# Performance work log

Hardware: AMD Instinct MI355X
Metric: run time of the kernel (lower is better)

Reference implementation:

```python
import jax, jax.numpy as jnp
import numpy as np

B, S, N, U, E, L = 32, 32, 128, 64, 2, 2
N_STEPS = 3
NUM_CLASSES = 5


def setup_inputs() -> dict:
    key = jax.random.key(0)
    ks = jax.random.split(key, 10)
    input_seq = jax.random.normal(ks[0], (B, S, N * U), dtype=jnp.float32)
    seq_lengths = jax.random.randint(ks[1], (B,), 0, S)
    # per-edge-type adjacency, scaled ~row-stochastic for numerical sanity
    adjacency_matrix = jax.random.uniform(ks[2], (B, E, N, N), dtype=jnp.float32) / N
    sc = 1.0 / np.sqrt(U)
    W_msg = jax.random.normal(ks[3], (L, E, U, U), dtype=jnp.float32) * sc
    b_msg = jnp.zeros((L, U), dtype=jnp.float32)
    Wg = jax.random.normal(ks[4], (L, 3, U, U), dtype=jnp.float32) * sc  # gates from aggregated messages
    Ug = jax.random.normal(ks[5], (L, 3, U, U), dtype=jnp.float32) * sc  # gates from hidden state
    bg = jnp.zeros((L, 3, U), dtype=jnp.float32)
    fc_w = jax.random.normal(ks[6], (U, NUM_CLASSES), dtype=jnp.float32) * sc
    fc_b = jnp.zeros((NUM_CLASSES,), dtype=jnp.float32)
    return {
        "input_seq": input_seq, "seq_lengths": seq_lengths,
        "adjacency_matrix": adjacency_matrix,
        "W_msg": W_msg, "b_msg": b_msg, "Wg": Wg, "Ug": Ug, "bg": bg,
        "fc_w": fc_w, "fc_b": fc_b,
    }


def _ggnn_layer(h, A, W_msg_l, b_msg_l, Wg_l, Ug_l, bg_l):
    # h: [S,B,N,U], A: [B,E,N,N] (shared across timesteps)
    for _ in range(N_STEPS):
        # typed message passing: sum_e A_e @ h @ W_e
        a = jnp.einsum('benm,sbmu,euv->sbnv', A, h, W_msg_l) + b_msg_l
        g_a = jnp.einsum('sbnu,guv->gsbnv', a, Wg_l)  # [3,S,B,N,U]
        z = jax.nn.sigmoid(g_a[0] + h @ Ug_l[0] + bg_l[0])
        r = jax.nn.sigmoid(g_a[1] + h @ Ug_l[1] + bg_l[1])
        c = jnp.tanh(g_a[2] + (r * h) @ Ug_l[2] + bg_l[2])
        h = (1.0 - z) * h + z * c
    return h


def reference(input_seq, seq_lengths, adjacency_matrix, W_msg, b_msg, Wg, Ug, bg, fc_w, fc_b):
    # encoder: hidden state is NOT carried across timesteps in the original
    # (cell is called with current input only), so timesteps are vectorized.
    cur = input_seq.reshape(B, S, N, U).transpose(1, 0, 2, 3)  # [S,B,N,U]
    for l in range(L):
        cur = _ggnn_layer(cur, adjacency_matrix, W_msg[l], b_msg[l], Wg[l], Ug[l], bg[l])
    out = cur.transpose(1, 0, 2, 3)  # [B,S,N,U]
    idx = jnp.clip(seq_lengths - 1, 0, S - 1)
    last = out[jnp.arange(B), idx]  # [B,N,U] (last relevant timestep)
    # dropout is identity in eval mode
    logits = jax.nn.relu(last) @ fc_w + fc_b  # [B,N,C]
    return jnp.max(logits, axis=1)  # [B,C]
```

## Files before the change

kernel.cpp:

```cpp
#include <hip/hip_runtime.h>

#define B 32
#define S 32
#define N 128
#define U 64
#define E 2
#define NCLS 5
#define RPW 4


__device__ __forceinline__ float sigmoid_f(float x) {
    return __fdividef(1.f, 1.f + __expf(-x));
}
__device__ __forceinline__ float tanh_f(float x) {
    float t = __expf(-2.f * fabsf(x));
    float y = __fdividef(1.f - t, 1.f + t);
    return copysignf(y, x);
}
__device__ __forceinline__ float bcast(float v, int u) {
    return __uint_as_float(__builtin_amdgcn_readlane(__float_as_uint(v), u));
}

template <int FIRST, int LAST>
__global__ __launch_bounds__(256) void k_step(
    const float* __restrict__ x, const int* __restrict__ lens,
    const float* __restrict__ hin, float* __restrict__ hout,
    const float* __restrict__ A, const float* __restrict__ Wmsg,
    const float* __restrict__ bmsg, const float* __restrict__ Wg,
    const float* __restrict__ Ug, const float* __restrict__ bg,
    const float* __restrict__ fcw, float* __restrict__ partial, int l) {
    __shared__ float red[4 * NCLS];
    int tid = threadIdx.x;
    int wave = tid >> 6, lane = tid & 63;
    int b = blockIdx.x >> 3;
    int q = blockIdx.x & 7;
    int n0 = __builtin_amdgcn_readfirstlane(q * 16 + wave * RPW);

    const float* __restrict__ hsrc;
    if (FIRST) {
        int idx = lens[b] - 1;
        idx = idx < 0 ? 0 : (idx > S - 1 ? S - 1 : idx);
        hsrc = x + (size_t)(b * S + idx) * N * U;
    } else {
        hsrc = hin + (size_t)b * N * U;
    }

    float hv[RPW];
#pragma unroll
    for (int r = 0; r < RPW; ++r) hv[r] = hsrc[(n0 + r) * U + lane];

    float s[RPW][E];
#pragma unroll
    for (int r = 0; r < RPW; ++r) { s[r][0] = 0.f; s[r][1] = 0.f; }
    {
        const float4* Ap[E][RPW];
#pragma unroll
        for (int e = 0; e < E; ++e)
#pragma unroll
            for (int r = 0; r < RPW; ++r)
                Ap[e][r] = (const float4*)(A + (((size_t)b * E + e) * N + n0 + r) * N);
#pragma unroll 2
        for (int m4 = 0; m4 < N / 4; ++m4) {
            float q0 = hsrc[(m4 * 4 + 0) * U + lane];
            float q1 = hsrc[(m4 * 4 + 1) * U + lane];
            float q2 = hsrc[(m4 * 4 + 2) * U + lane];
            float q3 = hsrc[(m4 * 4 + 3) * U + lane];
#pragma unroll
            for (int e = 0; e < E; ++e)
#pragma unroll
                for (int r = 0; r < RPW; ++r) {
                    float4 a = Ap[e][r][m4];
                    s[r][e] = fmaf(a.x, q0, s[r][e]);
                    s[r][e] = fmaf(a.y, q1, s[r][e]);
                    s[r][e] = fmaf(a.z, q2, s[r][e]);
                    s[r][e] = fmaf(a.w, q3, s[r][e]);
                }
        }
    }

    float bm = bmsg[l * U + lane];
    float av[RPW];
#pragma unroll
    for (int r = 0; r < RPW; ++r) av[r] = bm;
    {
        const float* W0 = Wmsg + (size_t)(l * E + 0) * U * U + lane;
        const float* W1 = W0 + U * U;
#pragma unroll 16
        for (int u = 0; u < U; ++u) {
            float w = W0[u * U];
#pragma unroll
            for (int r = 0; r < RPW; ++r) av[r] = fmaf(bcast(s[r][0], u), w, av[r]);
        }
#pragma unroll 16
        for (int u = 0; u < U; ++u) {
            float w = W1[u * U];
#pragma unroll
            for (int r = 0; r < RPW; ++r) av[r] = fmaf(bcast(s[r][1], u), w, av[r]);
        }
    }

    const float* Wg0 = Wg + (size_t)l * 3 * U * U + lane;
    const float* Wg1 = Wg0 + U * U;
    const float* Wg2 = Wg1 + U * U;
    const float* Ug0 = Ug + (size_t)l * 3 * U * U + lane;
    const float* Ug1 = Ug0 + U * U;
    const float* Ug2 = Ug1 + U * U;
    float bz = bg[(l * 3 + 0) * U + lane];
    float br = bg[(l * 3 + 1) * U + lane];
    float bcc = bg[(l * 3 + 2) * U + lane];
    float accz[RPW], accr[RPW], accc[RPW];
#pragma unroll
    for (int r = 0; r < RPW; ++r) { accz[r] = bz; accr[r] = br; accc[r] = bcc; }
#pragma unroll 8
    for (int u = 0; u < U; ++u) {
        float w0 = Wg0[u * U], w1 = Wg1[u * U], w2 = Wg2[u * U];
        float g0 = Ug0[u * U], g1 = Ug1[u * U];
#pragma unroll
        for (int r = 0; r < RPW; ++r) {
            float a = bcast(av[r], u);
            float h = bcast(hv[r], u);
            accz[r] = fmaf(a, w0, accz[r]); accz[r] = fmaf(h, g0, accz[r]);
            accr[r] = fmaf(a, w1, accr[r]); accr[r] = fmaf(h, g1, accr[r]);
            accc[r] = fmaf(a, w2, accc[r]);
        }
    }
    float rh[RPW];
#pragma unroll
    for (int r = 0; r < RPW; ++r) rh[r] = sigmoid_f(accr[r]) * hv[r];
#pragma unroll 16
    for (int u = 0; u < U; ++u) {
        float g2 = Ug2[u * U];
#pragma unroll
        for (int r = 0; r < RPW; ++r) accc[r] = fmaf(bcast(rh[r], u), g2, accc[r]);
    }
    float hn[RPW];
#pragma unroll
    for (int r = 0; r < RPW; ++r) {
        float zg = sigmoid_f(accz[r]);
        hn[r] = (1.f - zg) * hv[r] + zg * tanh_f(accc[r]);
    }

    if (!LAST) {
#pragma unroll
        for (int r = 0; r < RPW; ++r)
            hout[((size_t)b * N + n0 + r) * U + lane] = hn[r];
    } else {
        float lg[RPW][NCLS];
#pragma unroll
        for (int r = 0; r < RPW; ++r) {
            float rv = hn[r] > 0.f ? hn[r] : 0.f;
#pragma unroll
            for (int c = 0; c < NCLS; ++c) lg[r][c] = rv * fcw[lane * NCLS + c];
        }
#pragma unroll
        for (int off = 32; off; off >>= 1)
#pragma unroll
            for (int r = 0; r < RPW; ++r)
#pragma unroll
                for (int c = 0; c < NCLS; ++c) lg[r][c] += __shfl_xor(lg[r][c], off, 64);
        if (lane == 0) {
#pragma unroll
            for (int c = 0; c < NCLS; ++c)
                red[wave * NCLS + c] =
                    fmaxf(fmaxf(lg[0][c], lg[1][c]), fmaxf(lg[2][c], lg[3][c]));
        }
        __syncthreads();
        if (tid < NCLS) {
            float m = red[tid];
            for (int w = 1; w < 4; ++w) m = fmaxf(m, red[w * NCLS + tid]);
            partial[(size_t)(b * 8 + q) * NCLS + tid] = m;
        }
    }
}

__global__ void k_final(const float* __restrict__ partial, const float* __restrict__ fcb,
                        float* __restrict__ out) {
    int b = blockIdx.x, c = threadIdx.x;
    if (c < NCLS) {
        float m = -3.4e38f;
        for (int jj = 0; jj < 8; ++jj)
            m = fmaxf(m, partial[(size_t)(b * 8 + jj) * NCLS + c]);
        out[b * NCLS + c] = m + fcb[c];
    }
}

extern "C" void kernel_launch(void* const* d_in, const int* in_sizes, int n_in,
                              void* d_out, int out_size, void* d_ws, size_t ws_size,
                              hipStream_t stream) {
    const float* x    = (const float*)d_in[0];
    const int*   lens = (const int*)d_in[1];
    const float* A    = (const float*)d_in[2];
    const float* Wmsg = (const float*)d_in[3];
    const float* bmsg = (const float*)d_in[4];
    const float* Wg   = (const float*)d_in[5];
    const float* Ug   = (const float*)d_in[6];
    const float* bg   = (const float*)d_in[7];
    const float* fcw  = (const float*)d_in[8];
    const float* fcb  = (const float*)d_in[9];
    float* out = (float*)d_out;

    float* hA      = (float*)d_ws;
    float* hB      = hA + (size_t)B * N * U;
    float* partial = hB + (size_t)B * N * U;

    k_step<1, 0><<<B * 8, 256, 0, stream>>>(x, lens, nullptr, hA, A, Wmsg, bmsg, Wg, Ug, bg, fcw, partial, 0);
    k_step<0, 0><<<B * 8, 256, 0, stream>>>(x, lens, hA, hB, A, Wmsg, bmsg, Wg, Ug, bg, fcw, partial, 0);
    k_step<0, 0><<<B * 8, 256, 0, stream>>>(x, lens, hB, hA, A, Wmsg, bmsg, Wg, Ug, bg, fcw, partial, 0);
    k_step<0, 0><<<B * 8, 256, 0, stream>>>(x, lens, hA, hB, A, Wmsg, bmsg, Wg, Ug, bg, fcw, partial, 1);
    k_step<0, 0><<<B * 8, 256, 0, stream>>>(x, lens, hB, hA, A, Wmsg, bmsg, Wg, Ug, bg, fcw, partial, 1);
    k_step<0, 1><<<B * 8, 256, 0, stream>>>(x, lens, hA, hB, A, Wmsg, bmsg, Wg, Ug, bg, fcw, partial, 1);
    k_final<<<B, 64, 0, stream>>>(partial, fcb, out);
}
```

Before: 225.0 us.

## Split reductions across waves with LDS combine and pre-transposed float4 weights

Each block now covers 8 node rows, and its four waves split every reduction dimension four ways: the adjacency sum over m, and the sum over u in the message and gate matmuls. Partial sums are combined through shared memory with several barriers. The grid doubles to 512 blocks, and a new prep kernel transposes the weights into float4-packed layouts so each lane can load four weights at once. This shortens each wave's serial dependency chain and adds parallelism, at the cost of LDS traffic, extra __syncthreads, and an extra launch per call.

```diff
diff --git a/kernel.cpp b/kernel.cpp
--- a/kernel.cpp
+++ b/kernel.cpp
@@ -6,7 +6,6 @@
 #define U 64
 #define E 2
 #define NCLS 5
-#define RPW 4
 
 
 __device__ __forceinline__ float sigmoid_f(float x) {
@@ -21,20 +20,39 @@
     return __uint_as_float(__builtin_amdgcn_readlane(__float_as_uint(v), u));
 }
 
+__global__ __launch_bounds__(256) void k_prep(
+    const float* __restrict__ Wmsg, const float* __restrict__ Wg,
+    const float* __restrict__ Ug, float4* __restrict__ wt) {
+    int m = blockIdx.x;
+    const float* src;
+    if (m < 4)       src = Wmsg + (size_t)m * U * U;
+    else if (m < 10) src = Wg + (size_t)(m - 4) * U * U;
+    else             src = Ug + (size_t)(m - 10) * U * U;
+    for (int i = threadIdx.x; i < (U / 4) * U; i += 256) {
+        int u4 = i >> 6, v = i & 63;
+        wt[(size_t)m * 1024 + i] =
+            make_float4(src[(u4 * 4 + 0) * U + v], src[(u4 * 4 + 1) * U + v],
+                        src[(u4 * 4 + 2) * U + v], src[(u4 * 4 + 3) * U + v]);
+    }
+}
+
 template <int FIRST, int LAST>
-__global__ __launch_bounds__(256) void k_step(
+__global__ __launch_bounds__(256, 4) void k_step(
     const float* __restrict__ x, const int* __restrict__ lens,
     const float* __restrict__ hin, float* __restrict__ hout,
-    const float* __restrict__ A, const float* __restrict__ Wmsg,
-    const float* __restrict__ bmsg, const float* __restrict__ Wg,
-    const float* __restrict__ Ug, const float* __restrict__ bg,
+    const float* __restrict__ A, const float4* __restrict__ wt,
+    const float* __restrict__ bmsg, const float* __restrict__ bg,
     const float* __restrict__ fcw, float* __restrict__ partial, int l) {
-    __shared__ float red[4 * NCLS];
+    __shared__ float sA[4][8][2][64];
+    __shared__ float sB[4][8][64];
+    __shared__ float sC[4][8][64];
     int tid = threadIdx.x;
-    int wave = tid >> 6, lane = tid & 63;
-    int b = blockIdx.x >> 3;
-    int q = blockIdx.x & 7;
-    int n0 = __builtin_amdgcn_readfirstlane(q * 16 + wave * RPW);
+    int k = __builtin_amdgcn_readfirstlane(tid >> 6);
+    int lane = tid & 63;
+    int b = blockIdx.x >> 4;
+    int j = blockIdx.x & 15;
+    int n0 = __builtin_amdgcn_readfirstlane(j * 8);
+    int m0 = __builtin_amdgcn_readfirstlane(k * 32);
 
     const float* __restrict__ hsrc;
     if (FIRST) {
@@ -45,130 +63,200 @@
         hsrc = hin + (size_t)b * N * U;
     }
 
-    float hv[RPW];
-#pragma unroll
-    for (int r = 0; r < RPW; ++r) hv[r] = hsrc[(n0 + r) * U + lane];
-
-    float s[RPW][E];
-#pragma unroll
-    for (int r = 0; r < RPW; ++r) { s[r][0] = 0.f; s[r][1] = 0.f; }
+    float hv[8];
+#pragma unroll
+    for (int r = 0; r < 8; ++r) hv[r] = hsrc[(n0 + r) * U + lane];
+
+    float s2[8][2];
+#pragma unroll
+    for (int e = 0; e < E; ++e) {
+        float acc[8];
+#pragma unroll
+        for (int r = 0; r < 8; ++r) acc[r] = 0.f;
+        const float4* Ap[8];
+#pragma unroll
+        for (int r = 0; r < 8; ++r)
+            Ap[r] = (const float4*)(A + (((size_t)b * E + e) * N + n0 + r) * N + m0);
+#pragma unroll 2
+        for (int m4 = 0; m4 < 8; ++m4) {
+            float q0 = hsrc[(m0 + m4 * 4 + 0) * U + lane];
+            float q1 = hsrc[(m0 + m4 * 4 + 1) * U + lane];
+            float q2 = hsrc[(m0 + m4 * 4 + 2) * U + lane];
+            float q3 = hsrc[(m0 + m4 * 4 + 3) * U + lane];
+#pragma unroll
+            for (int r = 0; r < 8; ++r) {
+                float4 a = Ap[r][m4];
+                acc[r] = fmaf(a.x, q0, acc[r]);
+                acc[r] = fmaf(a.y, q1, acc[r]);
+                acc[r] = fmaf(a.z, q2, acc[r]);
+                acc[r] = fmaf(a.w, q3, acc[r]);
+            }
+        }
+#pragma unroll
+        for (int r = 0; r < 8; ++r) s2[r][e] = acc[r];
+    }
+#pragma unroll
+    for (int r = 0; r < 8; ++r) {
+        sA[k][r][0][lane] = s2[r][0];
+        sA[k][r][1][lane] = s2[r][1];
+    }
+    __syncthreads();
+#pragma unroll
+    for (int r = 0; r < 8; ++r) {
+        s2[r][0] = (sA[0][r][0][lane] + sA[1][r][0][lane]) + (sA[2][r][0][lane] + sA[3][r][0][lane]);
+        s2[r][1] = (sA[0][r][1][lane] + sA[1][r][1][lane]) + (sA[2][r][1][lane] + sA[3][r][1][lane]);
+    }
+
+    float av[8];
     {
-        const float4* Ap[E][RPW];
-#pragma unroll
-        for (int e = 0; e < E; ++e)
-#pragma unroll
-            for (int r = 0; r < RPW; ++r)
-                Ap[e][r] = (const float4*)(A + (((size_t)b * E + e) * N + n0 + r) * N);
-#pragma unroll 2
-        for (int m4 = 0; m4 < N / 4; ++m4) {
-            float q0 = hsrc[(m4 * 4 + 0) * U + lane];
-            float q1 = hsrc[(m4 * 4 + 1) * U + lane];
-            float q2 = hsrc[(m4 * 4 + 2) * U + lane];
-            float q3 = hsrc[(m4 * 4 + 3) * U + lane];
-#pragma unroll
-            for (int e = 0; e < E; ++e)
-#pragma unroll
-                for (int r = 0; r < RPW; ++r) {
-                    float4 a = Ap[e][r][m4];
-                    s[r][e] = fmaf(a.x, q0, s[r][e]);
-                    s[r][e] = fmaf(a.y, q1, s[r][e]);
-                    s[r][e] = fmaf(a.z, q2, s[r][e]);
-                    s[r][e] = fmaf(a.w, q3, s[r][e]);
+        float bm = (k == 0) ? bmsg[l * U + lane] : 0.f;
+#pragma unroll
+        for (int r = 0; r < 8; ++r) av[r] = bm;
+        const float4* W0t = wt + (size_t)(l * E + 0) * 1024 + lane;
+        const float4* W1t = W0t + 1024;
+#pragma unroll
+        for (int u4 = 0; u4 < 4; ++u4) {
+            float4 w4 = W0t[(k * 4 + u4) * 64];
+#pragma unroll
+            for (int i = 0; i < 4; ++i) {
+                int u = k * 16 + u4 * 4 + i;
+                float wv = ((const float*)&w4)[i];
+#pragma unroll
+                for (int r = 0; r < 8; ++r) av[r] = fmaf(bcast(s2[r][0], u), wv, av[r]);
+            }
+        }
+#pragma unroll
+        for (int u4 = 0; u4 < 4; ++u4) {
+            float4 w4 = W1t[(k * 4 + u4) * 64];
+#pragma unroll
+            for (int i = 0; i < 4; ++i) {
+                int u = k * 16 + u4 * 4 + i;
+                float wv = ((const float*)&w4)[i];
+#pragma unroll
+                for (int r = 0; r < 8; ++r) av[r] = fmaf(bcast(s2[r][1], u), wv, av[r]);
+            }
+        }
+    }
+#pragma unroll
+    for (int r = 0; r < 8; ++r) sB[k][r][lane] = av[r];
+    __syncthreads();
+#pragma unroll
+    for (int r = 0; r < 8; ++r)
+        av[r] = (sB[0][r][lane] + sB[1][r][lane]) + (sB[2][r][lane] + sB[3][r][lane]);
+
+    float accz[8], accr[8], accc[8];
+    {
+        float bz = (k == 0) ? bg[(l * 3 + 0) * U + lane] : 0.f;
+        float br = (k == 0) ? bg[(l * 3 + 1) * U + lane] : 0.f;
+        float bcc = (k == 0) ? bg[(l * 3 + 2) * U + lane] : 0.f;
+#pragma unroll
+        for (int r = 0; r < 8; ++r) { accz[r] = bz; accr[r] = br; accc[r] = bcc; }
+        const float4* Wg0t = wt + (size_t)(4 + l * 3 + 0) * 1024 + lane;
+        const float4* Wg1t = Wg0t + 1024;
+        const float4* Wg2t = Wg1t + 1024;
+        const float4* Ug0t = wt + (size_t)(10 + l * 3 + 0) * 1024 + lane;
+        const float4* Ug1t = Ug0t + 1024;
+#pragma unroll
+        for (int u4 = 0; u4 < 4; ++u4) {
+            float4 w0 = Wg0t[(k * 4 + u4) * 64];
+            float4 w1 = Wg1t[(k * 4 + u4) * 64];
+            float4 w2 = Wg2t[(k * 4 + u4) * 64];
+            float4 g0 = Ug0t[(k * 4 + u4) * 64];
+            float4 g1 = Ug1t[(k * 4 + u4) * 64];
+#pragma unroll
+            for (int i = 0; i < 4; ++i) {
+                int u = k * 16 + u4 * 4 + i;
+                float w0v = ((const float*)&w0)[i], w1v = ((const float*)&w1)[i];
+                float w2v = ((const float*)&w2)[i];
+                float g0v = ((const float*)&g0)[i], g1v = ((const float*)&g1)[i];
+#pragma unroll
+                for (int r = 0; r < 8; ++r) {
+                    float a = bcast(av[r], u);
+                    float h = bcast(hv[r], u);
+                    accz[r] = fmaf(a, w0v, accz[r]); accz[r] = fmaf(h, g0v, accz[r]);
+                    accr[r] = fmaf(a, w1v, accr[r]); accr[r] = fmaf(h, g1v, accr[r]);
+                    accc[r] = fmaf(a, w2v, accc[r]);
                 }
-        }
-    }
-
-    float bm = bmsg[l * U + lane];
-    float av[RPW];
-#pragma unroll
-    for (int r = 0; r < RPW; ++r) av[r] = bm;
+            }
+        }
+    }
+#pragma unroll
+    for (int r = 0; r < 8; ++r) {
+        sA[k][r][0][lane] = accz[r];
+        sA[k][r][1][lane] = accr[r];
+        sC[k][r][lane] = accc[r];
+    }
+    __syncthreads();
+#pragma unroll
+    for (int r = 0; r < 8; ++r) {
+        accz[r] = (sA[0][r][0][lane] + sA[1][r][0][lane]) + (sA[2][r][0][lane] + sA[3][r][0][lane]);
+        accr[r] = (sA[0][r][1][lane] + sA[1][r][1][lane]) + (sA[2][r][1][lane] + sA[3][r][1][lane]);
+        accc[r] = (sC[0][r][lane] + sC[1][r][lane]) + (sC[2][r][lane] + sC[3][r][lane]);
+    }
+
+    float rh[8];
+#pragma unroll
+    for (int r = 0; r < 8; ++r) rh[r] = sigmoid_f(accr[r]) * hv[r];
     {
-        const float* W0 = Wmsg + (size_t)(l * E + 0) * U * U + lane;
-        const float* W1 = W0 + U * U;
-#pragma unroll 16
-        for (int u = 0; u < U; ++u) {
-            float w = W0[u * U];
-#pragma unroll
-            for (int r = 0; r < RPW; ++r) av[r] = fmaf(bcast(s[r][0], u), w, av[r]);
-        }
-#pragma unroll 16
-        for (int u = 0; u < U; ++u) {
-            float w = W1[u * U];
-#pragma unroll
-            for (int r = 0; r < RPW; ++r) av[r] = fmaf(bcast(s[r][1], u), w, av[r]);
-        }
-    }
-
-    const float* Wg0 = Wg + (size_t)l * 3 * U * U + lane;
-    const float* Wg1 = Wg0 + U * U;
-    const float* Wg2 = Wg1 + U * U;
-    const float* Ug0 = Ug + (size_t)l * 3 * U * U + lane;
-    const float* Ug1 = Ug0 + U * U;
-    const float* Ug2 = Ug1 + U * U;
-    float bz = bg[(l * 3 + 0) * U + lane];
-    float br = bg[(l * 3 + 1) * U + lane];
-    float bcc = bg[(l * 3 + 2) * U + lane];
-    float accz[RPW], accr[RPW], accc[RPW];
-#pragma unroll
-    for (int r = 0; r < RPW; ++r) { accz[r] = bz; accr[r] = br; accc[r] = bcc; }
-#pragma unroll 8
-    for (int u = 0; u < U; ++u) {
-        float w0 = Wg0[u * U], w1 = Wg1[u * U], w2 = Wg2[u * U];
-        float g0 = Ug0[u * U], g1 = Ug1[u * U];
-#pragma unroll
-        for (int r = 0; r < RPW; ++r) {
-            float a = bcast(av[r], u);
-            float h = bcast(hv[r], u);
-            accz[r] = fmaf(a, w0, accz[r]); accz[r] = fmaf(h, g0, accz[r]);
-            accr[r] = fmaf(a, w1, accr[r]); accr[r] = fmaf(h, g1, accr[r]);
-            accc[r] = fmaf(a, w2, accc[r]);
-        }
-    }
-    float rh[RPW];
-#pragma unroll
-    for (int r = 0; r < RPW; ++r) rh[r] = sigmoid_f(accr[r]) * hv[r];
-#pragma unroll 16
-    for (int u = 0; u < U; ++u) {
-        float g2 = Ug2[u * U];
-#pragma unroll
-        for (int r = 0; r < RPW; ++r) accc[r] = fmaf(bcast(rh[r], u), g2, accc[r]);
-    }
-    float hn[RPW];
-#pragma unroll
-    for (int r = 0; r < RPW; ++r) {
+        const float4* Ug2t = wt + (size_t)(10 + l * 3 + 2) * 1024 + lane;
+        float c2[8];
+#pragma unroll
+        for (int r = 0; r < 8; ++r) c2[r] = 0.f;
+#pragma unroll
+        for (int u4 = 0; u4 < 4; ++u4) {
+            float4 g2 = Ug2t[(k * 4 + u4) * 64];
+#pragma unroll
+            for (int i = 0; i < 4; ++i) {
+                int u = k * 16 + u4 * 4 + i;
+                float g2v = ((const float*)&g2)[i];
+#pragma unroll
+                for (int r = 0; r < 8; ++r) c2[r] = fmaf(bcast(rh[r], u), g2v, c2[r]);
+            }
+        }
+#pragma unroll
+        for (int r = 0; r < 8; ++r) sB[k][r][lane] = c2[r];
+    }
+    __syncthreads();
+#pragma unroll
+    for (int r = 0; r < 8; ++r)
+        accc[r] += (sB[0][r][lane] + sB[1][r][lane]) + (sB[2][r][lane] + sB[3][r][lane]);
+
+    float hn[8];
+#pragma unroll
+    for (int r = 0; r < 8; ++r) {
         float zg = sigmoid_f(accz[r]);
         hn[r] = (1.f - zg) * hv[r] + zg * tanh_f(accc[r]);
     }
 
     if (!LAST) {
-#pragma unroll
-        for (int r = 0; r < RPW; ++r)
-            hout[((size_t)b * N + n0 + r) * U + lane] = hn[r];
+        if (k == 0) {
+#pragma unroll
+            for (int r = 0; r < 8; ++r)
+                hout[((size_t)b * N + n0 + r) * U + lane] = hn[r];
+        }
     } else {
-        float lg[RPW][NCLS];
-#pragma unroll
-        for (int r = 0; r < RPW; ++r) {
-            float rv = hn[r] > 0.f ? hn[r] : 0.f;
-#pragma unroll
-            for (int c = 0; c < NCLS; ++c) lg[r][c] = rv * fcw[lane * NCLS + c];
-        }
-#pragma unroll
-        for (int off = 32; off; off >>= 1)
-#pragma unroll
-            for (int r = 0; r < RPW; ++r)
-#pragma unroll
-                for (int c = 0; c < NCLS; ++c) lg[r][c] += __shfl_xor(lg[r][c], off, 64);
-        if (lane == 0) {
-#pragma unroll
-            for (int c = 0; c < NCLS; ++c)
-                red[wave * NCLS + c] =
-                    fmaxf(fmaxf(lg[0][c], lg[1][c]), fmaxf(lg[2][c], lg[3][c]));
-        }
-        __syncthreads();
-        if (tid < NCLS) {
-            float m = red[tid];
-            for (int w = 1; w < 4; ++w) m = fmaxf(m, red[w * NCLS + tid]);
-            partial[(size_t)(b * 8 + q) * NCLS + tid] = m;
+        if (k == 0) {
+            float mc[NCLS];
+#pragma unroll
+            for (int c = 0; c < NCLS; ++c) mc[c] = -3.4e38f;
+#pragma unroll
+            for (int r = 0; r < 8; ++r) {
+                float rv = hn[r] > 0.f ? hn[r] : 0.f;
+                float lg[NCLS];
+#pragma unroll
+                for (int c = 0; c < NCLS; ++c) lg[c] = rv * fcw[lane * NCLS + c];
+#pragma unroll
+                for (int off = 32; off; off >>= 1)
+#pragma unroll
+                    for (int c = 0; c < NCLS; ++c) lg[c] += __shfl_xor(lg[c], off, 64);
+#pragma unroll
+                for (int c = 0; c < NCLS; ++c) mc[c] = fmaxf(mc[c], lg[c]);
+            }
+            if (lane == 0) {
+#pragma unroll
+                for (int c = 0; c < NCLS; ++c)
+                    partial[(size_t)(b * 16 + j) * NCLS + c] = mc[c];
+            }
         }
     }
 }
@@ -178,8 +266,8 @@
     int b = blockIdx.x, c = threadIdx.x;
     if (c < NCLS) {
         float m = -3.4e38f;
-        for (int jj = 0; jj < 8; ++jj)
-            m = fmaxf(m, partial[(size_t)(b * 8 + jj) * NCLS + c]);
+        for (int jj = 0; jj < 16; ++jj)
+            m = fmaxf(m, partial[(size_t)(b * 16 + jj) * NCLS + c]);
         out[b * NCLS + c] = m + fcb[c];
     }
 }
@@ -202,12 +290,14 @@
     float* hA      = (float*)d_ws;
     float* hB      = hA + (size_t)B * N * U;
     float* partial = hB + (size_t)B * N * U;
-
-    k_step<1, 0><<<B * 8, 256, 0, stream>>>(x, lens, nullptr, hA, A, Wmsg, bmsg, Wg, Ug, bg, fcw, partial, 0);
-    k_step<0, 0><<<B * 8, 256, 0, stream>>>(x, lens, hA, hB, A, Wmsg, bmsg, Wg, Ug, bg, fcw, partial, 0);
-    k_step<0, 0><<<B * 8, 256, 0, stream>>>(x, lens, hB, hA, A, Wmsg, bmsg, Wg, Ug, bg, fcw, partial, 0);
-    k_step<0, 0><<<B * 8, 256, 0, stream>>>(x, lens, hA, hB, A, Wmsg, bmsg, Wg, Ug, bg, fcw, partial, 1);
-    k_step<0, 0><<<B * 8, 256, 0, stream>>>(x, lens, hB, hA, A, Wmsg, bmsg, Wg, Ug, bg, fcw, partial, 1);
-    k_step<0, 1><<<B * 8, 256, 0, stream>>>(x, lens, hA, hB, A, Wmsg, bmsg, Wg, Ug, bg, fcw, partial, 1);
+    float4* wt     = (float4*)(partial + (size_t)B * 16 * NCLS);
+
+    k_prep<<<16, 256, 0, stream>>>(Wmsg, Wg, Ug, wt);
+    k_step<1, 0><<<B * 16, 256, 0, stream>>>(x, lens, nullptr, hA, A, wt, bmsg, bg, fcw, partial, 0);
+    k_step<0, 0><<<B * 16, 256, 0, stream>>>(x, lens, hA, hB, A, wt, bmsg, bg, fcw, partial, 0);
+    k_step<0, 0><<<B * 16, 256, 0, stream>>>(x, lens, hB, hA, A, wt, bmsg, bg, fcw, partial, 0);
+    k_step<0, 0><<<B * 16, 256, 0, stream>>>(x, lens, hA, hB, A, wt, bmsg, bg, fcw, partial, 1);
+    k_step<0, 0><<<B * 16, 256, 0, stream>>>(x, lens, hB, hA, A, wt, bmsg, bg, fcw, partial, 1);
+    k_step<0, 1><<<B * 16, 256, 0, stream>>>(x, lens, hA, hB, A, wt, bmsg, bg, fcw, partial, 1);
     k_final<<<B, 64, 0, stream>>>(partial, fcb, out);
 }
```

New measurement: 205.4 us. 1.1x faster.
